# Kernel tuning notes

Hardware: AMD Instinct MI355X
Metric: run time of the kernel (lower is better)

## Reference

```python
import jax, jax.numpy as jnp
import numpy as np

BATCH = 2048
INPUT_DIM = 256
NUM_SUBCARRIERS = 256
HIDDEN_DIM = 256


def setup_inputs() -> dict:
    key = jax.random.key(0)
    ks = jax.random.split(key, 7)
    C, I, H = NUM_SUBCARRIERS, INPUT_DIM, HIDDEN_DIM
    # PyTorch nn.Linear default init: U(-1/sqrt(fan_in), 1/sqrt(fan_in))
    s1 = 1.0 / np.sqrt(I)
    s2 = 1.0 / np.sqrt(H)
    x = jax.random.normal(ks[0], (BATCH, I), dtype=jnp.float32)
    W1 = jax.random.uniform(ks[1], (C, I, H), jnp.float32, -s1, s1)
    b1 = jax.random.uniform(ks[2], (C, H), jnp.float32, -s1, s1)
    W2 = jax.random.uniform(ks[3], (C, H, H), jnp.float32, -s2, s2)
    b2 = jax.random.uniform(ks[4], (C, H), jnp.float32, -s2, s2)
    W3 = jax.random.uniform(ks[5], (C, H), jnp.float32, -s2, s2)  # [C, H] (out dim 1 squeezed)
    b3 = jax.random.uniform(ks[6], (C,), jnp.float32, -s2, s2)
    return {"x": x, "W1": W1, "b1": b1, "W2": W2, "b2": b2, "W3": W3, "b3": b3}


def reference(x, W1, b1, W2, b2, W3, b3):
    # Stacked (batched) version of the per-subcarrier Python loop:
    # for each subcarrier c: relu(relu(x @ W1[c] + b1[c]) @ W2[c] + b2[c]) @ W3[c] + b3[c]
    h1 = jax.nn.relu(jnp.einsum('bi,cih->cbh', x, W1) + b1[:, None, :])   # [C, B, H]
    h2 = jax.nn.relu(jnp.einsum('cbh,chk->cbk', h1, W2) + b2[:, None, :])  # [C, B, H]
    out = jnp.einsum('cbh,ch->cb', h2, W3) + b3[:, None]                   # [C, B]
    return out.T  # [B, C], matches torch.cat(outputs, dim=1)
```

## Files before the change

### kernel.cpp

```cpp
#include <hip/hip_runtime.h>

typedef unsigned short u16;
using u16x8  = __attribute__((ext_vector_type(8))) unsigned short;
using bf16x8 = __attribute__((ext_vector_type(8))) short;
using f32x16 = __attribute__((ext_vector_type(16))) float;

__device__ __forceinline__ u16 f2bf(float f) {
  union { float f; unsigned u; } v; v.f = f;
  unsigned r = v.u + 0x7FFFu + ((v.u >> 16) & 1u);
  return (u16)(r >> 16);
}

__global__ void convert_xA_k(const float* __restrict__ in, u16* __restrict__ out) {
  int flat = blockIdx.x * 256 + threadIdx.x;
  int b   = flat >> 5;
  int oct = flat & 31;
  const float4* src = (const float4*)(in + b * 256 + oct * 8);
  float4 v0 = src[0], v1 = src[1];
  u16x8 o;
  o[0] = f2bf(v0.x); o[1] = f2bf(v0.y); o[2] = f2bf(v0.z); o[3] = f2bf(v0.w);
  o[4] = f2bf(v1.x); o[5] = f2bf(v1.y); o[6] = f2bf(v1.z); o[7] = f2bf(v1.w);
  *(u16x8*)(out + ((b >> 5) << 13) + ((oct >> 1) << 9) + ((b & 31) << 4) + ((oct & 1) << 3)) = o;
}

__global__ __launch_bounds__(256) void transpose_w2_k(
    const float* __restrict__ W1, const float* __restrict__ W2,
    u16* __restrict__ w1t, u16* __restrict__ w2t) {
  __shared__ float tile[64][65];
  const int bid = blockIdx.x;
  const int mat = bid >> 4;
  const int tl  = bid & 15;
  const int i0 = (tl >> 2) * 64, h0 = (tl & 3) * 64;
  const float* src = (mat < 256) ? (W1 + mat * 65536) : (W2 + (mat - 256) * 65536);
  u16*       dst   = (mat < 256) ? (w1t + mat * 65536) : (w2t + (mat - 256) * 65536);
  const int t = threadIdx.x;
#pragma unroll
  for (int j = 0; j < 4; ++j) {
    int lin = j * 256 + t;
    int row = lin >> 4, c4 = lin & 15;
    float4 v = *(const float4*)(src + (i0 + row) * 256 + h0 + c4 * 4);
    tile[row][c4 * 4 + 0] = v.x; tile[row][c4 * 4 + 1] = v.y;
    tile[row][c4 * 4 + 2] = v.z; tile[row][c4 * 4 + 3] = v.w;
  }
  __syncthreads();
#pragma unroll
  for (int p = 0; p < 2; ++p) {
    int lin  = p * 256 + t;
    int nloc = lin >> 3;
    int oct  = lin & 7;
    u16x8 o;
#pragma unroll
    for (int jj = 0; jj < 8; ++jj)
      o[jj] = f2bf(tile[oct * 8 + jj][nloc]);
    *(u16x8*)(dst + ((i0 >> 4) + (oct >> 1)) * 4096 + (h0 + nloc) * 16 + (oct & 1) * 8) = o;
  }
}

__global__ __launch_bounds__(512, 4) void rf_main_k(
    const u16* __restrict__ xA, const u16* __restrict__ w1t, const u16* __restrict__ w2t,
    const float* __restrict__ b1, const float* __restrict__ b2,
    const float* __restrict__ w3, const float* __restrict__ b3,
    float* __restrict__ out) {
  __shared__ u16 sH1[128 * 264];
  __shared__ float red[512];

  const int bid  = blockIdx.x;
  const int xcd  = bid & 7;
  const int j8   = bid >> 3;
  const int c    = xcd * 32 + (j8 >> 4);
  const int b0   = (j8 & 15) * 128;
  const int t    = threadIdx.x;
  const int lane = t & 63;
  const int w    = t >> 6;
  const int l31  = lane & 31;
  const int hi   = lane >> 5;
  const int half = w >> 2;
  const int cb   = (w & 3) * 64;

  const u16* w1c = w1t + c * 65536;
  const u16* w2c = w2t + c * 65536;
  const int bBase = (cb + l31) * 16 + hi * 8;
  const int aBase = ((b0 >> 5) + half * 2) * 8192 + l31 * 16 + hi * 8;
  const int aLds  = (half * 64 + l31) * 264 + hi * 8;

  f32x16 acc[2][2] = {};
  bf16x8 a0[2], a1[2], bb0[2], bb1[2];

#define LOADA(dst, s)                                             \
  { _Pragma("unroll")                                             \
    for (int _m = 0; _m < 2; ++_m)                                \
      dst[_m] = *(const bf16x8*)(xA + aBase + _m * 8192 + (s) * 512); }
#define LOADB(dst, wc, s)                                         \
  { _Pragma("unroll")                                             \
    for (int _n = 0; _n < 2; ++_n)                                \
      dst[_n] = *(const bf16x8*)((wc) + bBase + _n * 512 + (s) * 4096); }
#define COMP_G(AA, BB)                                            \
  { _Pragma("unroll")                                             \
    for (int _m = 0; _m < 2; ++_m)                                \
      _Pragma("unroll")                                           \
      for (int _n = 0; _n < 2; ++_n)                              \
        acc[_m][_n] = __builtin_amdgcn_mfma_f32_32x32x16_bf16(AA[_m], BB[_n], acc[_m][_n], 0, 0, 0); }
#define COMP_L(BB, s)                                             \
  { bf16x8 _a[2];                                                 \
    _Pragma("unroll")                                             \
    for (int _m = 0; _m < 2; ++_m)                                \
      _a[_m] = *(const bf16x8*)&sH1[aLds + _m * (32 * 264) + (s) * 16]; \
    _Pragma("unroll")                                             \
    for (int _m = 0; _m < 2; ++_m)                                \
      _Pragma("unroll")                                           \
      for (int _n = 0; _n < 2; ++_n)                              \
        acc[_m][_n] = __builtin_amdgcn_mfma_f32_32x32x16_bf16(_a[_m], BB[_n], acc[_m][_n], 0, 0, 0); }

  LOADA(a0, 0); LOADB(bb0, w1c, 0);
#pragma unroll 1
  for (int s = 0; s < 14; s += 2) {
    LOADA(a1, s + 1); LOADB(bb1, w1c, s + 1);
    COMP_G(a0, bb0);
    LOADA(a0, s + 2); LOADB(bb0, w1c, s + 2);
    COMP_G(a1, bb1);
  }
  LOADA(a1, 15); LOADB(bb1, w1c, 15);
  COMP_G(a0, bb0);
  LOADB(bb0, w2c, 0);
  COMP_G(a1, bb1);

#pragma unroll
  for (int nt = 0; nt < 2; ++nt) {
    int col = cb + nt * 32 + l31;
    float bias = b1[c * 256 + col];
#pragma unroll
    for (int mt = 0; mt < 2; ++mt)
#pragma unroll
      for (int r = 0; r < 16; ++r) {
        int row = half * 64 + mt * 32 + (r & 3) + 8 * (r >> 2) + 4 * hi;
        float v = acc[mt][nt][r] + bias;
        v = v > 0.f ? v : 0.f;
        sH1[row * 264 + col] = f2bf(v);
        acc[mt][nt][r] = 0.f;
      }
  }
  __syncthreads();

#pragma unroll 1
  for (int s = 0; s < 14; s += 2) {
    LOADB(bb1, w2c, s + 1);
    COMP_L(bb0, s);
    LOADB(bb0, w2c, s + 2);
    COMP_L(bb1, s + 1);
  }
  LOADB(bb1, w2c, 15);
  COMP_L(bb0, 14);
  COMP_L(bb1, 15);

  float part[2][16];
#pragma unroll
  for (int mt = 0; mt < 2; ++mt)
#pragma unroll
    for (int r = 0; r < 16; ++r) part[mt][r] = 0.f;
#pragma unroll
  for (int nt = 0; nt < 2; ++nt) {
    int col = cb + nt * 32 + l31;
    float bias = b2[c * 256 + col];
    float w3v  = w3[c * 256 + col];
#pragma unroll
    for (int mt = 0; mt < 2; ++mt)
#pragma unroll
      for (int r = 0; r < 16; ++r) {
        float v = acc[mt][nt][r] + bias;
        v = v > 0.f ? v : 0.f;
        part[mt][r] += v * w3v;
      }
  }
#pragma unroll
  for (int m = 1; m < 32; m <<= 1)
#pragma unroll
    for (int mt = 0; mt < 2; ++mt)
#pragma unroll
      for (int r = 0; r < 16; ++r)
        part[mt][r] += __shfl_xor(part[mt][r], m, 64);

  if (l31 == 0) {
#pragma unroll
    for (int mt = 0; mt < 2; ++mt)
#pragma unroll
      for (int r = 0; r < 16; ++r) {
        int row = half * 64 + mt * 32 + (r & 3) + 8 * (r >> 2) + 4 * hi;
        red[(w & 3) * 128 + row] = part[mt][r];
      }
  }
  __syncthreads();
  if (t < 128) {
    float v = red[t] + red[128 + t] + red[256 + t] + red[384 + t] + b3[c];
    out[(b0 + t) * 256 + c] = v;
  }
#undef LOADA
#undef LOADB
#undef COMP_G
#undef COMP_L
}

extern "C" void kernel_launch(void* const* d_in, const int* in_sizes, int n_in,
                              void* d_out, int out_size, void* d_ws, size_t ws_size,
                              hipStream_t stream) {
  const float* x  = (const float*)d_in[0];
  const float* W1 = (const float*)d_in[1];
  const float* b1 = (const float*)d_in[2];
  const float* W2 = (const float*)d_in[3];
  const float* b2 = (const float*)d_in[4];
  const float* W3 = (const float*)d_in[5];
  const float* b3 = (const float*)d_in[6];
  float* out = (float*)d_out;

  char* ws = (char*)d_ws;
  u16* xA  = (u16*)ws;
  u16* w1t = (u16*)(ws + (1u << 20));
  u16* w2t = (u16*)(ws + (1u << 20) + (32u << 20));

  convert_xA_k  <<<256,  256, 0, stream>>>(x,  xA);
  transpose_w2_k<<<8192, 256, 0, stream>>>(W1, W2, w1t, w2t);
  rf_main_k     <<<4096, 512, 0, stream>>>(xA, w1t, w2t, b1, b2, W3, b3, out);
}
```

Baseline: 326.7 us.

## Stage x tile in LDS and fully unroll triple-buffered weight pipeline

The x conversion now writes plain row-major bf16, and the main kernel copies its 128-row x tile into shared memory. The first GEMM then reads A operands from LDS instead of global memory, matching the second GEMM. Both GEMM loops are fully unrolled with a three-deep register buffer for the weight fragments so global loads are issued further ahead of the MFMAs. The cost is an extra shared-memory fill plus a barrier per block, and higher register pressure from the extra buffers.

```diff
diff --git a/kernel.cpp b/kernel.cpp
--- a/kernel.cpp
+++ b/kernel.cpp
@@ -1,6 +1,7 @@
 #include <hip/hip_runtime.h>
 
 typedef unsigned short u16;
+using u16x4  = __attribute__((ext_vector_type(4))) unsigned short;
 using u16x8  = __attribute__((ext_vector_type(8))) unsigned short;
 using bf16x8 = __attribute__((ext_vector_type(8))) short;
 using f32x16 = __attribute__((ext_vector_type(16))) float;
@@ -11,16 +12,12 @@
   return (u16)(r >> 16);
 }
 
-__global__ void convert_xA_k(const float* __restrict__ in, u16* __restrict__ out) {
-  int flat = blockIdx.x * 256 + threadIdx.x;
-  int b   = flat >> 5;
-  int oct = flat & 31;
-  const float4* src = (const float4*)(in + b * 256 + oct * 8);
-  float4 v0 = src[0], v1 = src[1];
-  u16x8 o;
-  o[0] = f2bf(v0.x); o[1] = f2bf(v0.y); o[2] = f2bf(v0.z); o[3] = f2bf(v0.w);
-  o[4] = f2bf(v1.x); o[5] = f2bf(v1.y); o[6] = f2bf(v1.z); o[7] = f2bf(v1.w);
-  *(u16x8*)(out + ((b >> 5) << 13) + ((oct >> 1) << 9) + ((b & 31) << 4) + ((oct & 1) << 3)) = o;
+__global__ void convert_x_k(const float* __restrict__ in, u16* __restrict__ out) {
+  int i = blockIdx.x * 256 + threadIdx.x;
+  float4 v = ((const float4*)in)[i];
+  u16x4 u;
+  u.x = f2bf(v.x); u.y = f2bf(v.y); u.z = f2bf(v.z); u.w = f2bf(v.w);
+  ((u16x4*)out)[i] = u;
 }
 
 __global__ __launch_bounds__(256) void transpose_w2_k(
@@ -57,11 +54,11 @@
 }
 
 __global__ __launch_bounds__(512, 4) void rf_main_k(
-    const u16* __restrict__ xA, const u16* __restrict__ w1t, const u16* __restrict__ w2t,
+    const u16* __restrict__ xb, const u16* __restrict__ w1t, const u16* __restrict__ w2t,
     const float* __restrict__ b1, const float* __restrict__ b2,
     const float* __restrict__ w3, const float* __restrict__ b3,
     float* __restrict__ out) {
-  __shared__ u16 sH1[128 * 264];
+  __shared__ u16 sH[128 * 264];
   __shared__ float red[512];
 
   const int bid  = blockIdx.x;
@@ -80,50 +77,54 @@
   const u16* w1c = w1t + c * 65536;
   const u16* w2c = w2t + c * 65536;
   const int bBase = (cb + l31) * 16 + hi * 8;
-  const int aBase = ((b0 >> 5) + half * 2) * 8192 + l31 * 16 + hi * 8;
-  const int aLds  = (half * 64 + l31) * 264 + hi * 8;
+  const int aR    = (half * 64 + l31) * 264 + hi * 8;
 
   f32x16 acc[2][2] = {};
-  bf16x8 a0[2], a1[2], bb0[2], bb1[2];
-
-#define LOADA(dst, s)                                             \
-  { _Pragma("unroll")                                             \
-    for (int _m = 0; _m < 2; ++_m)                                \
-      dst[_m] = *(const bf16x8*)(xA + aBase + _m * 8192 + (s) * 512); }
-#define LOADB(dst, wc, s)                                         \
-  { _Pragma("unroll")                                             \
-    for (int _n = 0; _n < 2; ++_n)                                \
-      dst[_n] = *(const bf16x8*)((wc) + bBase + _n * 512 + (s) * 4096); }
-#define COMP_G(AA, BB)                                            \
-  { _Pragma("unroll")                                             \
-    for (int _m = 0; _m < 2; ++_m)                                \
-      _Pragma("unroll")                                           \
-      for (int _n = 0; _n < 2; ++_n)                              \
-        acc[_m][_n] = __builtin_amdgcn_mfma_f32_32x32x16_bf16(AA[_m], BB[_n], acc[_m][_n], 0, 0, 0); }
-#define COMP_L(BB, s)                                             \
-  { bf16x8 _a[2];                                                 \
-    _Pragma("unroll")                                             \
-    for (int _m = 0; _m < 2; ++_m)                                \
-      _a[_m] = *(const bf16x8*)&sH1[aLds + _m * (32 * 264) + (s) * 16]; \
-    _Pragma("unroll")                                             \
-    for (int _m = 0; _m < 2; ++_m)                                \
-      _Pragma("unroll")                                           \
-      for (int _n = 0; _n < 2; ++_n)                              \
-        acc[_m][_n] = __builtin_amdgcn_mfma_f32_32x32x16_bf16(_a[_m], BB[_n], acc[_m][_n], 0, 0, 0); }
-
-  LOADA(a0, 0); LOADB(bb0, w1c, 0);
-#pragma unroll 1
-  for (int s = 0; s < 14; s += 2) {
-    LOADA(a1, s + 1); LOADB(bb1, w1c, s + 1);
-    COMP_G(a0, bb0);
-    LOADA(a0, s + 2); LOADB(bb0, w1c, s + 2);
-    COMP_G(a1, bb1);
-  }
-  LOADA(a1, 15); LOADB(bb1, w1c, 15);
-  COMP_G(a0, bb0);
-  LOADB(bb0, w2c, 0);
-  COMP_G(a1, bb1);
-
+  bf16x8 a[2][2], bb[3][2];
+
+#define BL(i, wc, s)                                                     \
+  { bb[i][0] = *(const bf16x8*)((wc) + bBase + (s) * 4096);              \
+    bb[i][1] = *(const bf16x8*)((wc) + bBase + 512 + (s) * 4096); }
+#define AL(ai, s)                                                        \
+  { a[ai][0] = *(const bf16x8*)&sH[aR + (s) * 16];                       \
+    a[ai][1] = *(const bf16x8*)&sH[aR + 32 * 264 + (s) * 16]; }
+#define MM(ai, bi)                                                       \
+  { _Pragma("unroll")                                                    \
+    for (int _m = 0; _m < 2; ++_m)                                       \
+      _Pragma("unroll")                                                  \
+      for (int _n = 0; _n < 2; ++_n)                                     \
+        acc[_m][_n] = __builtin_amdgcn_mfma_f32_32x32x16_bf16(           \
+            a[ai][_m], bb[bi][_n], acc[_m][_n], 0, 0, 0); }
+
+  BL(0, w1c, 0); BL(1, w1c, 1);
+
+#pragma unroll
+  for (int i = 0; i < 8; ++i) {
+    int flat = i * 512 + t;
+    int r = flat >> 5, s = flat & 31;
+    *(u16x8*)&sH[r * 264 + s * 8] = *(const u16x8*)(xb + (b0 + r) * 256 + s * 8);
+  }
+  __syncthreads();
+
+  AL(0, 0);
+  BL(2, w1c, 2);  AL(1, 1);  MM(0, 0);
+  BL(0, w1c, 3);  AL(0, 2);  MM(1, 1);
+  BL(1, w1c, 4);  AL(1, 3);  MM(0, 2);
+  BL(2, w1c, 5);  AL(0, 4);  MM(1, 0);
+  BL(0, w1c, 6);  AL(1, 5);  MM(0, 1);
+  BL(1, w1c, 7);  AL(0, 6);  MM(1, 2);
+  BL(2, w1c, 8);  AL(1, 7);  MM(0, 0);
+  BL(0, w1c, 9);  AL(0, 8);  MM(1, 1);
+  BL(1, w1c, 10); AL(1, 9);  MM(0, 2);
+  BL(2, w1c, 11); AL(0, 10); MM(1, 0);
+  BL(0, w1c, 12); AL(1, 11); MM(0, 1);
+  BL(1, w1c, 13); AL(0, 12); MM(1, 2);
+  BL(2, w1c, 14); AL(1, 13); MM(0, 0);
+  BL(0, w1c, 15); AL(0, 14); MM(1, 1);
+  BL(1, w2c, 0);  AL(1, 15); MM(0, 2);
+  BL(2, w2c, 1);             MM(1, 0);
+
+  __syncthreads();
 #pragma unroll
   for (int nt = 0; nt < 2; ++nt) {
     int col = cb + nt * 32 + l31;
@@ -135,22 +136,29 @@
         int row = half * 64 + mt * 32 + (r & 3) + 8 * (r >> 2) + 4 * hi;
         float v = acc[mt][nt][r] + bias;
         v = v > 0.f ? v : 0.f;
-        sH1[row * 264 + col] = f2bf(v);
+        sH[row * 264 + col] = f2bf(v);
         acc[mt][nt][r] = 0.f;
       }
   }
   __syncthreads();
 
-#pragma unroll 1
-  for (int s = 0; s < 14; s += 2) {
-    LOADB(bb1, w2c, s + 1);
-    COMP_L(bb0, s);
-    LOADB(bb0, w2c, s + 2);
-    COMP_L(bb1, s + 1);
-  }
-  LOADB(bb1, w2c, 15);
-  COMP_L(bb0, 14);
-  COMP_L(bb1, 15);
+  AL(0, 0);
+  BL(0, w2c, 2);  AL(1, 1);  MM(0, 1);
+  BL(1, w2c, 3);  AL(0, 2);  MM(1, 2);
+  BL(2, w2c, 4);  AL(1, 3);  MM(0, 0);
+  BL(0, w2c, 5);  AL(0, 4);  MM(1, 1);
+  BL(1, w2c, 6);  AL(1, 5);  MM(0, 2);
+  BL(2, w2c, 7);  AL(0, 6);  MM(1, 0);
+  BL(0, w2c, 8);  AL(1, 7);  MM(0, 1);
+  BL(1, w2c, 9);  AL(0, 8);  MM(1, 2);
+  BL(2, w2c, 10); AL(1, 9);  MM(0, 0);
+  BL(0, w2c, 11); AL(0, 10); MM(1, 1);
+  BL(1, w2c, 12); AL(1, 11); MM(0, 2);
+  BL(2, w2c, 13); AL(0, 12); MM(1, 0);
+  BL(0, w2c, 14); AL(1, 13); MM(0, 1);
+  BL(1, w2c, 15); AL(0, 14); MM(1, 2);
+                  AL(1, 15); MM(0, 0);
+                             MM(1, 1);
 
   float part[2][16];
 #pragma unroll
@@ -193,10 +201,9 @@
     float v = red[t] + red[128 + t] + red[256 + t] + red[384 + t] + b3[c];
     out[(b0 + t) * 256 + c] = v;
   }
-#undef LOADA
-#undef LOADB
-#undef COMP_G
-#undef COMP_L
+#undef BL
+#undef AL
+#undef MM
 }
 
 extern "C" void kernel_launch(void* const* d_in, const int* in_sizes, int n_in,
@@ -212,11 +219,11 @@
   float* out = (float*)d_out;
 
   char* ws = (char*)d_ws;
-  u16* xA  = (u16*)ws;
+  u16* xb  = (u16*)ws;
   u16* w1t = (u16*)(ws + (1u << 20));
   u16* w2t = (u16*)(ws + (1u << 20) + (32u << 20));
 
-  convert_xA_k  <<<256,  256, 0, stream>>>(x,  xA);
+  convert_x_k   <<<512,  256, 0, stream>>>(x,  xb);
   transpose_w2_k<<<8192, 256, 0, stream>>>(W1, W2, w1t, w2t);
-  rf_main_k     <<<4096, 512, 0, stream>>>(xA, w1t, w2t, b1, b2, W3, b3, out);
-}
+  rf_main_k     <<<4096, 512, 0, stream>>>(xb, w1t, w2t, b1, b2, W3, b3, out);
+}
```

After: 325.7 us. Within noise of the previous version (-0.3%).
